# Optimization experiments

Hardware: AMD Instinct MI355X
Metric: run time of the kernel (lower is better)

## Reference

```python
import jax, jax.numpy as jnp
import numpy as np

MASK_PENALTY = 10000.0

def setup_inputs() -> dict:
    key = jax.random.key(0)
    kq, kk, kv = jax.random.split(key, 3)
    B, S, D = 8, 2048, 64
    return {
        "query": jax.random.normal(kq, (B, S, D), dtype=jnp.float32),
        "key": jax.random.normal(kk, (B, S, D), dtype=jnp.float32),
        "value": jax.random.normal(kv, (B, S, D), dtype=jnp.float32),
        "mask": jnp.ones((B, S), dtype=jnp.bool_),
    }

def reference(query, key, value, mask):
    # e: [B, Sq, Sk]
    d = query.shape[-1]
    e = jnp.einsum('bqd,bkd->bqk', query, key) / jnp.sqrt(jnp.float32(d))
    Sq, Sk = query.shape[1], key.shape[1]
    # history_only causal mask: key index > query index gets -10000
    causal = (jnp.arange(Sk)[None, :] > jnp.arange(Sq)[:, None]).astype(jnp.float32)
    e = e - MASK_PENALTY * causal[None, :, :]
    # padding mask: [B, Sk] -> [B, 1, Sk]
    e = e - MASK_PENALTY * (1.0 - mask.astype(jnp.float32))[:, None, :]
    attn = jax.nn.softmax(e, axis=-1)
    return jnp.einsum('bqk,bkd->bqd', attn, value)
```

## Files before the change

### kernel.cpp

```cpp
#include <hip/hip_runtime.h>


typedef _Float16 f16x8 __attribute__((ext_vector_type(8)));
typedef _Float16 f16x4 __attribute__((ext_vector_type(4)));
typedef float    f32x4 __attribute__((ext_vector_type(4)));

#define MFMA_K32(A, B, C) __builtin_amdgcn_mfma_f32_16x16x32_f16(A, B, C, 0, 0, 0)
#define MFMA_K16(A, B, C) __builtin_amdgcn_mfma_f32_16x16x16f16(A, B, C, 0, 0, 0)

__device__ inline unsigned pack2h(float a, float b) {
    union { _Float16 h[2]; unsigned u; } t;
    t.h[0] = (_Float16)a; t.h[1] = (_Float16)b;
    return t.u;
}

constexpr float CSCALE = 0.18033688011112042f;

__global__ __launch_bounds__(256, 4)
void prep_f16(const float* __restrict__ K, const float* __restrict__ V,
              const int* __restrict__ M, _Float16* __restrict__ Kh,
              _Float16* __restrict__ Vq, unsigned char* __restrict__ Mb) {
    __shared__ _Float16 sT[64 * 80];
    const int b   = blockIdx.x >> 5;
    const int s0  = (blockIdx.x & 31) * 64;
    const int t   = threadIdx.x;
    const int row = t >> 2;
    const int grp = (t & 3) * 16;
    const size_t base = ((size_t)b * 2048 + s0 + row) * 64 + grp;
    {
        union { _Float16 h[16]; f16x8 v[2]; } o;
        const float* p = K + base;
#pragma unroll
        for (int i = 0; i < 16; i += 4) {
            float4 x = *(const float4*)(p + i);
            o.h[i]   = (_Float16)(x.x * CSCALE); o.h[i+1] = (_Float16)(x.y * CSCALE);
            o.h[i+2] = (_Float16)(x.z * CSCALE); o.h[i+3] = (_Float16)(x.w * CSCALE);
        }
        *(f16x8*)(Kh + base) = o.v[0];
        *(f16x8*)(Kh + base + 8) = o.v[1];
    }
    {
        const float* p = V + base;
#pragma unroll
        for (int i = 0; i < 16; i += 4) {
            float4 x = *(const float4*)(p + i);
            sT[(grp + i    ) * 80 + row] = (_Float16)x.x;
            sT[(grp + i + 1) * 80 + row] = (_Float16)x.y;
            sT[(grp + i + 2) * 80 + row] = (_Float16)x.z;
            sT[(grp + i + 3) * 80 + row] = (_Float16)x.w;
        }
    }
    if (t < 64) {
        const size_t s = (size_t)b * 2048 + s0 + t;
        Mb[s] = (unsigned char)(M[s] != 0);
    }
    __syncthreads();
    {
        const int d = t & 63, g = t >> 6;
        const size_t o = (((size_t)b * 128 + (s0 >> 4) + g) * 64 + d) * 16;
        *(f16x8*)(Vq + o)     = *(const f16x8*)&sT[d * 80 + g * 16];
        *(f16x8*)(Vq + o + 8) = *(const f16x8*)&sT[d * 80 + g * 16 + 8];
    }
}

constexpr int SOSTR = 68;

__global__ __launch_bounds__(512, 2)
void attn_f16_v6(const float* __restrict__ Q, const _Float16* __restrict__ Kh,
                 const _Float16* __restrict__ Vq, const unsigned char* __restrict__ Mb,
                 float* __restrict__ O) {
    constexpr int S = 2048, D = 64;

    __shared__ float sO[8][32 * SOSTR];
    __shared__ float sL[8][32];

    const int tid  = threadIdx.x;
    const int w    = tid >> 6;
    const int lane = tid & 63;
    const int l15  = lane & 15;
    const int quad = lane >> 4;

    for (int phase = 0; phase < 2; ++phase) {
        const int batch = (int)blockIdx.y ^ phase;
        const int st    = phase ? 63 - (int)blockIdx.x : (int)blockIdx.x;
        const int n_kt  = st + 1;
        const int qg0   = st * 32;
        const size_t bq = (size_t)batch * S;
        const _Float16* Kb = Kh + bq * D;
        const _Float16* Vb = Vq + bq * D;

        f16x8 qf[2][2];
#pragma unroll
        for (int f = 0; f < 2; ++f) {
            const float* qp = Q + (bq + qg0 + f * 16 + l15) * D + quad * 8;
#pragma unroll
            for (int dc = 0; dc < 2; ++dc) {
                float4 x0 = *(const float4*)(qp + dc * 32);
                float4 x1 = *(const float4*)(qp + dc * 32 + 4);
                union { unsigned u[4]; f16x8 v; } t;
                t.u[0] = pack2h(x0.x, x0.y); t.u[1] = pack2h(x0.z, x0.w);
                t.u[2] = pack2h(x1.x, x1.y); t.u[3] = pack2h(x1.z, x1.w);
                qf[f][dc] = t.v;
            }
        }

        f32x4 acc[2][4];
        float lacc[2] = {0.f, 0.f};
#pragma unroll
        for (int f = 0; f < 2; ++f)
#pragma unroll
            for (int c = 0; c < 4; ++c) { acc[f][c][0] = acc[f][c][1] = acc[f][c][2] = acc[f][c][3] = 0.f; }

        f16x8 kn[2][2];
        if (w < n_kt) {
            const int kb = w * 32;
#pragma unroll
            for (int kg = 0; kg < 2; ++kg)
#pragma unroll
                for (int dc = 0; dc < 2; ++dc)
                    kn[kg][dc] = *(const f16x8*)(Kb + (size_t)(kb + kg * 16 + l15) * D + dc * 32 + quad * 8);
        }

        for (int t = w; t < n_kt; t += 8) {
            const int kb = t * 32;

            f16x4 vf[2][4];
#pragma unroll
            for (int kg = 0; kg < 2; ++kg)
#pragma unroll
                for (int c = 0; c < 4; ++c)
                    vf[kg][c] = *(const f16x4*)(Vb + ((size_t)((kb >> 4) + kg) * 64 + c * 16 + l15) * 16 + quad * 4);
            const unsigned um0 = *(const unsigned*)(Mb + bq + kb + quad * 4);
            const unsigned um1 = *(const unsigned*)(Mb + bq + kb + 16 + quad * 4);

            f32x4 scT[2][2];
#pragma unroll
            for (int f = 0; f < 2; ++f) {
                f32x4 z; z[0] = z[1] = z[2] = z[3] = 0.f;
                f32x4 y0 = MFMA_K32(kn[0][0], qf[f][0], z);
                scT[f][0] = MFMA_K32(kn[0][1], qf[f][1], y0);
                f32x4 y1 = MFMA_K32(kn[1][0], qf[f][0], z);
                scT[f][1] = MFMA_K32(kn[1][1], qf[f][1], y1);
            }

            if (t + 8 < n_kt) {
                const int kb2 = kb + 256;
#pragma unroll
                for (int kg = 0; kg < 2; ++kg)
#pragma unroll
                    for (int dc = 0; dc < 2; ++dc)
                        kn[kg][dc] = *(const f16x8*)(Kb + (size_t)(kb2 + kg * 16 + l15) * D + dc * 32 + quad * 8);
            }

#pragma unroll
            for (int f = 0; f < 2; ++f) {
                const int qrow = qg0 + f * 16 + l15;
                f16x4 pf0, pf1;
                {
                    union { _Float16 h[4]; f16x4 v; } pp;
#pragma unroll
                    for (int r = 0; r < 4; ++r) {
                        const int key = kb + quad * 4 + r;
                        float e  = __builtin_amdgcn_exp2f(scT[f][0][r]);
                        bool  ok = (key <= qrow) && (((um0 >> (8 * r)) & 0xFF) != 0);
                        float pv = ok ? e : 0.f;
                        lacc[f] += pv;
                        pp.h[r] = (_Float16)pv;
                    }
                    pf0 = pp.v;
#pragma unroll
                    for (int r = 0; r < 4; ++r) {
                        const int key = kb + 16 + quad * 4 + r;
                        float e  = __builtin_amdgcn_exp2f(scT[f][1][r]);
                        bool  ok = (key <= qrow) && (((um1 >> (8 * r)) & 0xFF) != 0);
                        float pv = ok ? e : 0.f;
                        lacc[f] += pv;
                        pp.h[r] = (_Float16)pv;
                    }
                    pf1 = pp.v;
                }
                acc[f][0] = MFMA_K16(pf0, vf[0][0], acc[f][0]);
                acc[f][1] = MFMA_K16(pf0, vf[0][1], acc[f][1]);
                acc[f][2] = MFMA_K16(pf0, vf[0][2], acc[f][2]);
                acc[f][3] = MFMA_K16(pf0, vf[0][3], acc[f][3]);
                acc[f][0] = MFMA_K16(pf1, vf[1][0], acc[f][0]);
                acc[f][1] = MFMA_K16(pf1, vf[1][1], acc[f][1]);
                acc[f][2] = MFMA_K16(pf1, vf[1][2], acc[f][2]);
                acc[f][3] = MFMA_K16(pf1, vf[1][3], acc[f][3]);
            }
        }

#pragma unroll
        for (int f = 0; f < 2; ++f) {
            lacc[f] += __shfl_xor(lacc[f], 16, 64);
            lacc[f] += __shfl_xor(lacc[f], 32, 64);
        }

#pragma unroll
        for (int f = 0; f < 2; ++f)
#pragma unroll
            for (int c = 0; c < 4; ++c)
#pragma unroll
                for (int r = 0; r < 4; ++r)
                    sO[w][(f * 16 + quad * 4 + r) * SOSTR + c * 16 + l15] = acc[f][c][r];
        if (lane < 16) { sL[w][l15] = lacc[0]; sL[w][16 + l15] = lacc[1]; }
        __syncthreads();
        {
            const int row = tid >> 4;
            const int col = (tid & 15) * 4;
            float a0 = 0.f, a1 = 0.f, a2 = 0.f, a3 = 0.f, l = 0.f;
#pragma unroll
            for (int w2 = 0; w2 < 8; ++w2) {
                const float* p = &sO[w2][row * SOSTR + col];
                a0 += p[0]; a1 += p[1]; a2 += p[2]; a3 += p[3];
                l  += sL[w2][row];
            }
            const float inv = 1.f / fmaxf(l, 1e-37f);
            float4 o; o.x = a0 * inv; o.y = a1 * inv; o.z = a2 * inv; o.w = a3 * inv;
            *(float4*)(&O[(bq + qg0 + row) * D + col]) = o;
        }
        __syncthreads();
    }
}

constexpr int PSTR = 40;
__global__ __launch_bounds__(512, 4)
void attn_f16_slow(const float* __restrict__ Q, const float* __restrict__ K,
                   const float* __restrict__ V, const int* __restrict__ M,
                   float* __restrict__ O) {
    constexpr int S = 2048, D = 64;
    __shared__ __align__(16) _Float16 sP[8][16 * PSTR];
    __shared__ float sO[8][16 * 64];
    __shared__ float sL[8][16];
    const int tid = threadIdx.x, w = tid >> 6, lane = tid & 63;
    const int l15 = lane & 15, quad = lane >> 4;
    for (int phase = 0; phase < 2; ++phase) {
        const int batch = (int)blockIdx.y ^ phase;
        const int tile  = phase ? 127 - (int)blockIdx.x : (int)blockIdx.x;
        const int n_kt  = tile / 2 + 1;
        const int qg0   = tile * 16;
        const size_t bq = (size_t)batch * S;
        f16x8 qf[2];
        {
            const float* qp = Q + (bq + qg0 + l15) * D + quad * 8;
#pragma unroll
            for (int dc = 0; dc < 2; ++dc) {
                float4 x0 = *(const float4*)(qp + dc * 32);
                float4 x1 = *(const float4*)(qp + dc * 32 + 4);
                union { unsigned u[4]; f16x8 v; } t;
                t.u[0] = pack2h(x0.x, x0.y); t.u[1] = pack2h(x0.z, x0.w);
                t.u[2] = pack2h(x1.x, x1.y); t.u[3] = pack2h(x1.z, x1.w);
                qf[dc] = t.v;
            }
        }
        f32x4 acc[4]; float lacc[4];
#pragma unroll
        for (int c = 0; c < 4; ++c) { acc[c][0] = acc[c][1] = acc[c][2] = acc[c][3] = 0.f; }
#pragma unroll
        for (int r = 0; r < 4; ++r) lacc[r] = 0.f;
        for (int t = w; t < n_kt; t += 8) {
            const int kb = t * 32;
            f16x8 kf[2][2];
            {
                const float* kp = K + (bq + kb + l15) * D + quad * 8;
#pragma unroll
                for (int kg = 0; kg < 2; ++kg)
#pragma unroll
                    for (int dc = 0; dc < 2; ++dc) {
                        float4 x0 = *(const float4*)(kp + kg * 16 * D + dc * 32);
                        float4 x1 = *(const float4*)(kp + kg * 16 * D + dc * 32 + 4);
                        union { unsigned u[4]; f16x8 v; } tt;
                        tt.u[0] = pack2h(x0.x * CSCALE, x0.y * CSCALE);
                        tt.u[1] = pack2h(x0.z * CSCALE, x0.w * CSCALE);
                        tt.u[2] = pack2h(x1.x * CSCALE, x1.y * CSCALE);
                        tt.u[3] = pack2h(x1.z * CSCALE, x1.w * CSCALE);
                        kf[kg][dc] = tt.v;
                    }
            }
            float vr[4][8];
            {
                const float* vp = V + (bq + kb + quad * 8) * D + l15;
#pragma unroll
                for (int c = 0; c < 4; ++c)
#pragma unroll
                    for (int j = 0; j < 8; ++j)
                        vr[c][j] = vp[j * D + c * 16];
            }
            const int m0 = M[bq + kb + l15];
            const int m1 = M[bq + kb + 16 + l15];
            f32x4 sc[2];
#pragma unroll
            for (int kg = 0; kg < 2; ++kg) {
                f32x4 z; z[0] = z[1] = z[2] = z[3] = 0.f;
                z = MFMA_K32(qf[0], kf[kg][0], z);
                sc[kg] = MFMA_K32(qf[1], kf[kg][1], z);
            }
            float p[2][4];
#pragma unroll
            for (int kg = 0; kg < 2; ++kg) {
                const int key = kb + kg * 16 + l15;
                const int mv  = kg ? m1 : m0;
#pragma unroll
                for (int r = 0; r < 4; ++r) {
                    const int qrow = qg0 + quad * 4 + r;
                    float e  = __builtin_amdgcn_exp2f(sc[kg][r]);
                    bool  ok = (key <= qrow) && (mv != 0);
                    float pv = ok ? e : 0.f;
                    p[kg][r] = pv;
                    lacc[r] += pv;
                }
            }
            _Float16* sPw = sP[w];
#pragma unroll
            for (int kg = 0; kg < 2; ++kg)
#pragma unroll
                for (int r = 0; r < 4; ++r)
                    sPw[(quad * 4 + r) * PSTR + kg * 16 + l15] = (_Float16)p[kg][r];
            f16x8 pf = *(const f16x8*)(&sPw[l15 * PSTR + quad * 8]);
#pragma unroll
            for (int c = 0; c < 4; ++c) {
                union { unsigned u[4]; f16x8 v; } tt;
                tt.u[0] = pack2h(vr[c][0], vr[c][1]);
                tt.u[1] = pack2h(vr[c][2], vr[c][3]);
                tt.u[2] = pack2h(vr[c][4], vr[c][5]);
                tt.u[3] = pack2h(vr[c][6], vr[c][7]);
                acc[c] = MFMA_K32(pf, tt.v, acc[c]);
            }
        }
#pragma unroll
        for (int r = 0; r < 4; ++r) {
            float s = lacc[r];
            s += __shfl_xor(s, 1, 64);
            s += __shfl_xor(s, 2, 64);
            s += __shfl_xor(s, 4, 64);
            s += __shfl_xor(s, 8, 64);
            lacc[r] = s;
        }
#pragma unroll
        for (int c = 0; c < 4; ++c)
#pragma unroll
            for (int r = 0; r < 4; ++r)
                sO[w][(quad * 4 + r) * 64 + c * 16 + l15] = acc[c][r];
        if (l15 == 0) {
#pragma unroll
            for (int r = 0; r < 4; ++r) sL[w][quad * 4 + r] = lacc[r];
        }
        __syncthreads();
        {
            const int row = tid >> 5;
            const int col = (tid & 31) * 2;
            float a = 0.f, b = 0.f, l = 0.f;
#pragma unroll
            for (int w2 = 0; w2 < 8; ++w2) {
                a += sO[w2][row * 64 + col];
                b += sO[w2][row * 64 + col + 1];
                l += sL[w2][row];
            }
            const float inv = 1.f / fmaxf(l, 1e-37f);
            float2 o; o.x = a * inv; o.y = b * inv;
            *(float2*)(&O[(bq + qg0 + row) * D + col]) = o;
        }
        __syncthreads();
    }
}

extern "C" void kernel_launch(void* const* d_in, const int* in_sizes, int n_in,
                              void* d_out, int out_size, void* d_ws, size_t ws_size,
                              hipStream_t stream) {
    const float* Q = (const float*)d_in[0];
    const float* K = (const float*)d_in[1];
    const float* V = (const float*)d_in[2];
    const int*   M = (const int*)d_in[3];
    float*       O = (float*)d_out;
    const size_t n_kv = (size_t)8 * 2048 * 64;
    const size_t need = n_kv * 2 * sizeof(_Float16) + 8 * 2048;
    if (ws_size >= need) {
        _Float16* Kh = (_Float16*)d_ws;
        _Float16* Vq = Kh + n_kv;
        unsigned char* Mb = (unsigned char*)(Vq + n_kv);
        hipLaunchKernelGGL(prep_f16, dim3(256), dim3(256), 0, stream, K, V, M, Kh, Vq, Mb);
        hipLaunchKernelGGL(attn_f16_v6, dim3(32, 8), dim3(512), 0, stream, Q, Kh, Vq, Mb, O);
    } else {
        hipLaunchKernelGGL(attn_f16_slow, dim3(64, 8), dim3(512), 0, stream, Q, K, V, M, O);
    }
}
```

Before: 85.76 us.

## Double-buffer K/V/mask tiles in registers and use additive float mask bias

Replaces the single K-prefetch with two register slots holding K, V and mask for alternating tiles, so loads for the next-next tile overlap compute on the current one. The padding mask becomes a precomputed additive float bias (0 or -1e5) folded into the exp2 argument, removing the per-element byte extraction and compare. The causal compare now runs only on diagonal tiles. This raises register pressure under launch bounds of 512x2, which could cause spills or lower occupancy.

```diff
diff --git a/kernel.cpp b/kernel.cpp
--- a/kernel.cpp
+++ b/kernel.cpp
@@ -19,7 +19,7 @@
 __global__ __launch_bounds__(256, 4)
 void prep_f16(const float* __restrict__ K, const float* __restrict__ V,
               const int* __restrict__ M, _Float16* __restrict__ Kh,
-              _Float16* __restrict__ Vq, unsigned char* __restrict__ Mb) {
+              _Float16* __restrict__ Vq, float* __restrict__ Mf) {
     __shared__ _Float16 sT[64 * 80];
     const int b   = blockIdx.x >> 5;
     const int s0  = (blockIdx.x & 31) * 64;
@@ -52,7 +52,7 @@
     }
     if (t < 64) {
         const size_t s = (size_t)b * 2048 + s0 + t;
-        Mb[s] = (unsigned char)(M[s] != 0);
+        Mf[s] = M[s] ? 0.f : -1.0e5f;
     }
     __syncthreads();
     {
@@ -65,9 +65,15 @@
 
 constexpr int SOSTR = 68;
 
+struct Slot {
+    f16x8 kf[2][2];
+    f16x4 vf[2][4];
+    float mb[2][4];
+};
+
 __global__ __launch_bounds__(512, 2)
-void attn_f16_v6(const float* __restrict__ Q, const _Float16* __restrict__ Kh,
-                 const _Float16* __restrict__ Vq, const unsigned char* __restrict__ Mb,
+void attn_f16_v7(const float* __restrict__ Q, const _Float16* __restrict__ Kh,
+                 const _Float16* __restrict__ Vq, const float* __restrict__ Mf,
                  float* __restrict__ O) {
     constexpr int S = 2048, D = 64;
 
@@ -88,6 +94,7 @@
         const size_t bq = (size_t)batch * S;
         const _Float16* Kb = Kh + bq * D;
         const _Float16* Vb = Vq + bq * D;
+        const float*    Mb = Mf + bq;
 
         f16x8 qf[2][2];
 #pragma unroll
@@ -111,82 +118,82 @@
 #pragma unroll
             for (int c = 0; c < 4; ++c) { acc[f][c][0] = acc[f][c][1] = acc[f][c][2] = acc[f][c][3] = 0.f; }
 
-        f16x8 kn[2][2];
-        if (w < n_kt) {
-            const int kb = w * 32;
+        auto fill = [&](Slot& s, int kb) {
 #pragma unroll
             for (int kg = 0; kg < 2; ++kg)
 #pragma unroll
                 for (int dc = 0; dc < 2; ++dc)
-                    kn[kg][dc] = *(const f16x8*)(Kb + (size_t)(kb + kg * 16 + l15) * D + dc * 32 + quad * 8);
-        }
-
-        for (int t = w; t < n_kt; t += 8) {
-            const int kb = t * 32;
-
-            f16x4 vf[2][4];
+                    s.kf[kg][dc] = *(const f16x8*)(Kb + (size_t)(kb + kg * 16 + l15) * D + dc * 32 + quad * 8);
 #pragma unroll
             for (int kg = 0; kg < 2; ++kg)
 #pragma unroll
                 for (int c = 0; c < 4; ++c)
-                    vf[kg][c] = *(const f16x4*)(Vb + ((size_t)((kb >> 4) + kg) * 64 + c * 16 + l15) * 16 + quad * 4);
-            const unsigned um0 = *(const unsigned*)(Mb + bq + kb + quad * 4);
-            const unsigned um1 = *(const unsigned*)(Mb + bq + kb + 16 + quad * 4);
-
+                    s.vf[kg][c] = *(const f16x4*)(Vb + ((size_t)((kb >> 4) + kg) * 64 + c * 16 + l15) * 16 + quad * 4);
+#pragma unroll
+            for (int kg = 0; kg < 2; ++kg) {
+                float4 m = *(const float4*)(Mb + kb + kg * 16 + quad * 4);
+                s.mb[kg][0] = m.x; s.mb[kg][1] = m.y; s.mb[kg][2] = m.z; s.mb[kg][3] = m.w;
+            }
+        };
+
+        auto compute_tile = [&](const Slot& s, int kb) {
             f32x4 scT[2][2];
 #pragma unroll
             for (int f = 0; f < 2; ++f) {
                 f32x4 z; z[0] = z[1] = z[2] = z[3] = 0.f;
-                f32x4 y0 = MFMA_K32(kn[0][0], qf[f][0], z);
-                scT[f][0] = MFMA_K32(kn[0][1], qf[f][1], y0);
-                f32x4 y1 = MFMA_K32(kn[1][0], qf[f][0], z);
-                scT[f][1] = MFMA_K32(kn[1][1], qf[f][1], y1);
-            }
-
-            if (t + 8 < n_kt) {
-                const int kb2 = kb + 256;
-#pragma unroll
-                for (int kg = 0; kg < 2; ++kg)
-#pragma unroll
-                    for (int dc = 0; dc < 2; ++dc)
-                        kn[kg][dc] = *(const f16x8*)(Kb + (size_t)(kb2 + kg * 16 + l15) * D + dc * 32 + quad * 8);
-            }
-
+                f32x4 y0 = MFMA_K32(s.kf[0][0], qf[f][0], z);
+                scT[f][0] = MFMA_K32(s.kf[0][1], qf[f][1], y0);
+                f32x4 y1 = MFMA_K32(s.kf[1][0], qf[f][0], z);
+                scT[f][1] = MFMA_K32(s.kf[1][1], qf[f][1], y1);
+            }
+            const bool causal = (kb + 32 > qg0);
 #pragma unroll
             for (int f = 0; f < 2; ++f) {
                 const int qrow = qg0 + f * 16 + l15;
                 f16x4 pf0, pf1;
-                {
-                    union { _Float16 h[4]; f16x4 v; } pp;
-#pragma unroll
-                    for (int r = 0; r < 4; ++r) {
+                union { _Float16 h[4]; f16x4 v; } pp;
+#pragma unroll
+                for (int r = 0; r < 4; ++r) {
+                    float e = __builtin_amdgcn_exp2f(scT[f][0][r] + s.mb[0][r]);
+                    if (causal) {
                         const int key = kb + quad * 4 + r;
-                        float e  = __builtin_amdgcn_exp2f(scT[f][0][r]);
-                        bool  ok = (key <= qrow) && (((um0 >> (8 * r)) & 0xFF) != 0);
-                        float pv = ok ? e : 0.f;
-                        lacc[f] += pv;
-                        pp.h[r] = (_Float16)pv;
+                        e = (key <= qrow) ? e : 0.f;
                     }
-                    pf0 = pp.v;
-#pragma unroll
-                    for (int r = 0; r < 4; ++r) {
+                    lacc[f] += e;
+                    pp.h[r] = (_Float16)e;
+                }
+                pf0 = pp.v;
+#pragma unroll
+                for (int r = 0; r < 4; ++r) {
+                    float e = __builtin_amdgcn_exp2f(scT[f][1][r] + s.mb[1][r]);
+                    if (causal) {
                         const int key = kb + 16 + quad * 4 + r;
-                        float e  = __builtin_amdgcn_exp2f(scT[f][1][r]);
-                        bool  ok = (key <= qrow) && (((um1 >> (8 * r)) & 0xFF) != 0);
-                        float pv = ok ? e : 0.f;
-                        lacc[f] += pv;
-                        pp.h[r] = (_Float16)pv;
+                        e = (key <= qrow) ? e : 0.f;
                     }
-                    pf1 = pp.v;
+                    lacc[f] += e;
+                    pp.h[r] = (_Float16)e;
                 }
-                acc[f][0] = MFMA_K16(pf0, vf[0][0], acc[f][0]);
-                acc[f][1] = MFMA_K16(pf0, vf[0][1], acc[f][1]);
-                acc[f][2] = MFMA_K16(pf0, vf[0][2], acc[f][2]);
-                acc[f][3] = MFMA_K16(pf0, vf[0][3], acc[f][3]);
-                acc[f][0] = MFMA_K16(pf1, vf[1][0], acc[f][0]);
-                acc[f][1] = MFMA_K16(pf1, vf[1][1], acc[f][1]);
-                acc[f][2] = MFMA_K16(pf1, vf[1][2], acc[f][2]);
-                acc[f][3] = MFMA_K16(pf1, vf[1][3], acc[f][3]);
+                pf1 = pp.v;
+                acc[f][0] = MFMA_K16(pf0, s.vf[0][0], acc[f][0]);
+                acc[f][1] = MFMA_K16(pf0, s.vf[0][1], acc[f][1]);
+                acc[f][2] = MFMA_K16(pf0, s.vf[0][2], acc[f][2]);
+                acc[f][3] = MFMA_K16(pf0, s.vf[0][3], acc[f][3]);
+                acc[f][0] = MFMA_K16(pf1, s.vf[1][0], acc[f][0]);
+                acc[f][1] = MFMA_K16(pf1, s.vf[1][1], acc[f][1]);
+                acc[f][2] = MFMA_K16(pf1, s.vf[1][2], acc[f][2]);
+                acc[f][3] = MFMA_K16(pf1, s.vf[1][3], acc[f][3]);
+            }
+        };
+
+        Slot s0, s1;
+        if (w < n_kt)     fill(s0, w * 32);
+        if (w + 8 < n_kt) fill(s1, (w + 8) * 32);
+        for (int t = w; t < n_kt; t += 16) {
+            compute_tile(s0, t * 32);
+            if (t + 16 < n_kt) fill(s0, (t + 16) * 32);
+            if (t + 8 < n_kt) {
+                compute_tile(s1, (t + 8) * 32);
+                if (t + 24 < n_kt) fill(s1, (t + 24) * 32);
             }
         }
 
@@ -373,13 +380,13 @@
     const int*   M = (const int*)d_in[3];
     float*       O = (float*)d_out;
     const size_t n_kv = (size_t)8 * 2048 * 64;
-    const size_t need = n_kv * 2 * sizeof(_Float16) + 8 * 2048;
+    const size_t need = n_kv * 2 * sizeof(_Float16) + (size_t)8 * 2048 * sizeof(float);
     if (ws_size >= need) {
         _Float16* Kh = (_Float16*)d_ws;
         _Float16* Vq = Kh + n_kv;
-        unsigned char* Mb = (unsigned char*)(Vq + n_kv);
-        hipLaunchKernelGGL(prep_f16, dim3(256), dim3(256), 0, stream, K, V, M, Kh, Vq, Mb);
-        hipLaunchKernelGGL(attn_f16_v6, dim3(32, 8), dim3(512), 0, stream, Q, Kh, Vq, Mb, O);
+        float*    Mf = (float*)(Vq + n_kv);
+        hipLaunchKernelGGL(prep_f16, dim3(256), dim3(256), 0, stream, K, V, M, Kh, Vq, Mf);
+        hipLaunchKernelGGL(attn_f16_v7, dim3(32, 8), dim3(512), 0, stream, Q, Kh, Vq, Mf, O);
     } else {
         hipLaunchKernelGGL(attn_f16_slow, dim3(64, 8), dim3(512), 0, stream, Q, K, V, M, O);
     }
```

New measurement: 88.26 us. +2.9%, slower.

## Split attention into 16-row query tiles with 4 waves and additive mask bias

Applied to the files above, without the earlier changes.

Replaces the two-phase paired 32-row blocks of 8 waves with 1024 independent 256-thread blocks. Each block handles 16 query rows, ordered longest-first so the causal load balances across more, smaller blocks. The padding mask becomes a precomputed float additive bias folded into the exponent, and the causal compare runs only on diagonal tiles. This cuts per-element masking ALU work and raises occupancy, at the cost of reloading K/V for every 16 rows instead of every 32 and a larger mask buffer.

```diff
diff --git a/kernel.cpp b/kernel.cpp
--- a/kernel.cpp
+++ b/kernel.cpp
@@ -19,7 +19,7 @@
 __global__ __launch_bounds__(256, 4)
 void prep_f16(const float* __restrict__ K, const float* __restrict__ V,
               const int* __restrict__ M, _Float16* __restrict__ Kh,
-              _Float16* __restrict__ Vq, unsigned char* __restrict__ Mb) {
+              _Float16* __restrict__ Vq, float* __restrict__ Mf) {
     __shared__ _Float16 sT[64 * 80];
     const int b   = blockIdx.x >> 5;
     const int s0  = (blockIdx.x & 31) * 64;
@@ -52,7 +52,7 @@
     }
     if (t < 64) {
         const size_t s = (size_t)b * 2048 + s0 + t;
-        Mb[s] = (unsigned char)(M[s] != 0);
+        Mf[s] = M[s] ? 0.f : -1.0e5f;
     }
     __syncthreads();
     {
@@ -65,14 +65,14 @@
 
 constexpr int SOSTR = 68;
 
-__global__ __launch_bounds__(512, 2)
-void attn_f16_v6(const float* __restrict__ Q, const _Float16* __restrict__ Kh,
-                 const _Float16* __restrict__ Vq, const unsigned char* __restrict__ Mb,
+__global__ __launch_bounds__(256, 4)
+void attn_f16_v8(const float* __restrict__ Q, const _Float16* __restrict__ Kh,
+                 const _Float16* __restrict__ Vq, const float* __restrict__ Mf,
                  float* __restrict__ O) {
     constexpr int S = 2048, D = 64;
 
-    __shared__ float sO[8][32 * SOSTR];
-    __shared__ float sL[8][32];
+    __shared__ float sO[4][16 * SOSTR];
+    __shared__ float sL[4][16];
 
     const int tid  = threadIdx.x;
     const int w    = tid >> 6;
@@ -80,146 +80,139 @@
     const int l15  = lane & 15;
     const int quad = lane >> 4;
 
-    for (int phase = 0; phase < 2; ++phase) {
-        const int batch = (int)blockIdx.y ^ phase;
-        const int st    = phase ? 63 - (int)blockIdx.x : (int)blockIdx.x;
-        const int n_kt  = st + 1;
-        const int qg0   = st * 32;
-        const size_t bq = (size_t)batch * S;
-        const _Float16* Kb = Kh + bq * D;
-        const _Float16* Vb = Vq + bq * D;
-
-        f16x8 qf[2][2];
-#pragma unroll
-        for (int f = 0; f < 2; ++f) {
-            const float* qp = Q + (bq + qg0 + f * 16 + l15) * D + quad * 8;
-#pragma unroll
-            for (int dc = 0; dc < 2; ++dc) {
-                float4 x0 = *(const float4*)(qp + dc * 32);
-                float4 x1 = *(const float4*)(qp + dc * 32 + 4);
-                union { unsigned u[4]; f16x8 v; } t;
-                t.u[0] = pack2h(x0.x, x0.y); t.u[1] = pack2h(x0.z, x0.w);
-                t.u[2] = pack2h(x1.x, x1.y); t.u[3] = pack2h(x1.z, x1.w);
-                qf[f][dc] = t.v;
-            }
-        }
-
-        f32x4 acc[2][4];
-        float lacc[2] = {0.f, 0.f};
-#pragma unroll
-        for (int f = 0; f < 2; ++f)
-#pragma unroll
-            for (int c = 0; c < 4; ++c) { acc[f][c][0] = acc[f][c][1] = acc[f][c][2] = acc[f][c][3] = 0.f; }
-
-        f16x8 kn[2][2];
-        if (w < n_kt) {
-            const int kb = w * 32;
+    const int idx   = (int)blockIdx.x;
+    const int tile  = 127 - (idx >> 3);
+    const int batch = idx & 7;
+    const int n_kt  = tile / 2 + 1;
+    const int qg0   = tile * 16;
+    const size_t bq = (size_t)batch * S;
+    const _Float16* Kb = Kh + bq * D;
+    const _Float16* Vb = Vq + bq * D;
+    const float*    Mb = Mf + bq;
+
+    f16x8 qf[2];
+    {
+        const float* qp = Q + (bq + qg0 + l15) * D + quad * 8;
+#pragma unroll
+        for (int dc = 0; dc < 2; ++dc) {
+            float4 x0 = *(const float4*)(qp + dc * 32);
+            float4 x1 = *(const float4*)(qp + dc * 32 + 4);
+            union { unsigned u[4]; f16x8 v; } t;
+            t.u[0] = pack2h(x0.x, x0.y); t.u[1] = pack2h(x0.z, x0.w);
+            t.u[2] = pack2h(x1.x, x1.y); t.u[3] = pack2h(x1.z, x1.w);
+            qf[dc] = t.v;
+        }
+    }
+
+    f32x4 acc[4];
+    float lacc = 0.f;
+#pragma unroll
+    for (int c = 0; c < 4; ++c) { acc[c][0] = acc[c][1] = acc[c][2] = acc[c][3] = 0.f; }
+
+    f16x8 kn[2][2];
+    if (w < n_kt) {
+        const int kb = w * 32;
+#pragma unroll
+        for (int kg = 0; kg < 2; ++kg)
+#pragma unroll
+            for (int dc = 0; dc < 2; ++dc)
+                kn[kg][dc] = *(const f16x8*)(Kb + (size_t)(kb + kg * 16 + l15) * D + dc * 32 + quad * 8);
+    }
+
+    for (int t = w; t < n_kt; t += 4) {
+        const int kb = t * 32;
+
+        f16x4 vf[2][4];
+#pragma unroll
+        for (int kg = 0; kg < 2; ++kg)
+#pragma unroll
+            for (int c = 0; c < 4; ++c)
+                vf[kg][c] = *(const f16x4*)(Vb + ((size_t)((kb >> 4) + kg) * 64 + c * 16 + l15) * 16 + quad * 4);
+        float4 mbias0 = *(const float4*)(Mb + kb + quad * 4);
+        float4 mbias1 = *(const float4*)(Mb + kb + 16 + quad * 4);
+
+        f32x4 scT0, scT1;
+        {
+            f32x4 z; z[0] = z[1] = z[2] = z[3] = 0.f;
+            f32x4 y0 = MFMA_K32(kn[0][0], qf[0], z);
+            scT0 = MFMA_K32(kn[0][1], qf[1], y0);
+            f32x4 y1 = MFMA_K32(kn[1][0], qf[0], z);
+            scT1 = MFMA_K32(kn[1][1], qf[1], y1);
+        }
+
+        if (t + 4 < n_kt) {
+            const int kb2 = kb + 128;
 #pragma unroll
             for (int kg = 0; kg < 2; ++kg)
 #pragma unroll
                 for (int dc = 0; dc < 2; ++dc)
-                    kn[kg][dc] = *(const f16x8*)(Kb + (size_t)(kb + kg * 16 + l15) * D + dc * 32 + quad * 8);
-        }
-
-        for (int t = w; t < n_kt; t += 8) {
-            const int kb = t * 32;
-
-            f16x4 vf[2][4];
-#pragma unroll
-            for (int kg = 0; kg < 2; ++kg)
-#pragma unroll
-                for (int c = 0; c < 4; ++c)
-                    vf[kg][c] = *(const f16x4*)(Vb + ((size_t)((kb >> 4) + kg) * 64 + c * 16 + l15) * 16 + quad * 4);
-            const unsigned um0 = *(const unsigned*)(Mb + bq + kb + quad * 4);
-            const unsigned um1 = *(const unsigned*)(Mb + bq + kb + 16 + quad * 4);
-
-            f32x4 scT[2][2];
-#pragma unroll
-            for (int f = 0; f < 2; ++f) {
-                f32x4 z; z[0] = z[1] = z[2] = z[3] = 0.f;
-                f32x4 y0 = MFMA_K32(kn[0][0], qf[f][0], z);
-                scT[f][0] = MFMA_K32(kn[0][1], qf[f][1], y0);
-                f32x4 y1 = MFMA_K32(kn[1][0], qf[f][0], z);
-                scT[f][1] = MFMA_K32(kn[1][1], qf[f][1], y1);
-            }
-
-            if (t + 8 < n_kt) {
-                const int kb2 = kb + 256;
-#pragma unroll
-                for (int kg = 0; kg < 2; ++kg)
-#pragma unroll
-                    for (int dc = 0; dc < 2; ++dc)
-                        kn[kg][dc] = *(const f16x8*)(Kb + (size_t)(kb2 + kg * 16 + l15) * D + dc * 32 + quad * 8);
-            }
-
-#pragma unroll
-            for (int f = 0; f < 2; ++f) {
-                const int qrow = qg0 + f * 16 + l15;
-                f16x4 pf0, pf1;
-                {
-                    union { _Float16 h[4]; f16x4 v; } pp;
-#pragma unroll
-                    for (int r = 0; r < 4; ++r) {
-                        const int key = kb + quad * 4 + r;
-                        float e  = __builtin_amdgcn_exp2f(scT[f][0][r]);
-                        bool  ok = (key <= qrow) && (((um0 >> (8 * r)) & 0xFF) != 0);
-                        float pv = ok ? e : 0.f;
-                        lacc[f] += pv;
-                        pp.h[r] = (_Float16)pv;
-                    }
-                    pf0 = pp.v;
-#pragma unroll
-                    for (int r = 0; r < 4; ++r) {
-                        const int key = kb + 16 + quad * 4 + r;
-                        float e  = __builtin_amdgcn_exp2f(scT[f][1][r]);
-                        bool  ok = (key <= qrow) && (((um1 >> (8 * r)) & 0xFF) != 0);
-                        float pv = ok ? e : 0.f;
-                        lacc[f] += pv;
-                        pp.h[r] = (_Float16)pv;
-                    }
-                    pf1 = pp.v;
+                    kn[kg][dc] = *(const f16x8*)(Kb + (size_t)(kb2 + kg * 16 + l15) * D + dc * 32 + quad * 8);
+        }
+
+        const bool diag = (kb + 32 > qg0);
+        const int qrow = qg0 + l15;
+        f16x4 pf0, pf1;
+        {
+            union { _Float16 h[4]; f16x4 v; } pp;
+            const float mb0[4] = {mbias0.x, mbias0.y, mbias0.z, mbias0.w};
+#pragma unroll
+            for (int r = 0; r < 4; ++r) {
+                float e = __builtin_amdgcn_exp2f(scT0[r] + mb0[r]);
+                if (diag) {
+                    const int key = kb + quad * 4 + r;
+                    e = (key <= qrow) ? e : 0.f;
                 }
-                acc[f][0] = MFMA_K16(pf0, vf[0][0], acc[f][0]);
-                acc[f][1] = MFMA_K16(pf0, vf[0][1], acc[f][1]);
-                acc[f][2] = MFMA_K16(pf0, vf[0][2], acc[f][2]);
-                acc[f][3] = MFMA_K16(pf0, vf[0][3], acc[f][3]);
-                acc[f][0] = MFMA_K16(pf1, vf[1][0], acc[f][0]);
-                acc[f][1] = MFMA_K16(pf1, vf[1][1], acc[f][1]);
-                acc[f][2] = MFMA_K16(pf1, vf[1][2], acc[f][2]);
-                acc[f][3] = MFMA_K16(pf1, vf[1][3], acc[f][3]);
-            }
-        }
-
-#pragma unroll
-        for (int f = 0; f < 2; ++f) {
-            lacc[f] += __shfl_xor(lacc[f], 16, 64);
-            lacc[f] += __shfl_xor(lacc[f], 32, 64);
-        }
-
-#pragma unroll
-        for (int f = 0; f < 2; ++f)
-#pragma unroll
-            for (int c = 0; c < 4; ++c)
-#pragma unroll
-                for (int r = 0; r < 4; ++r)
-                    sO[w][(f * 16 + quad * 4 + r) * SOSTR + c * 16 + l15] = acc[f][c][r];
-        if (lane < 16) { sL[w][l15] = lacc[0]; sL[w][16 + l15] = lacc[1]; }
-        __syncthreads();
-        {
-            const int row = tid >> 4;
-            const int col = (tid & 15) * 4;
-            float a0 = 0.f, a1 = 0.f, a2 = 0.f, a3 = 0.f, l = 0.f;
-#pragma unroll
-            for (int w2 = 0; w2 < 8; ++w2) {
-                const float* p = &sO[w2][row * SOSTR + col];
-                a0 += p[0]; a1 += p[1]; a2 += p[2]; a3 += p[3];
-                l  += sL[w2][row];
-            }
-            const float inv = 1.f / fmaxf(l, 1e-37f);
-            float4 o; o.x = a0 * inv; o.y = a1 * inv; o.z = a2 * inv; o.w = a3 * inv;
-            *(float4*)(&O[(bq + qg0 + row) * D + col]) = o;
-        }
-        __syncthreads();
+                lacc += e;
+                pp.h[r] = (_Float16)e;
+            }
+            pf0 = pp.v;
+            const float mb1[4] = {mbias1.x, mbias1.y, mbias1.z, mbias1.w};
+#pragma unroll
+            for (int r = 0; r < 4; ++r) {
+                float e = __builtin_amdgcn_exp2f(scT1[r] + mb1[r]);
+                if (diag) {
+                    const int key = kb + 16 + quad * 4 + r;
+                    e = (key <= qrow) ? e : 0.f;
+                }
+                lacc += e;
+                pp.h[r] = (_Float16)e;
+            }
+            pf1 = pp.v;
+        }
+
+        acc[0] = MFMA_K16(pf0, vf[0][0], acc[0]);
+        acc[1] = MFMA_K16(pf0, vf[0][1], acc[1]);
+        acc[2] = MFMA_K16(pf0, vf[0][2], acc[2]);
+        acc[3] = MFMA_K16(pf0, vf[0][3], acc[3]);
+        acc[0] = MFMA_K16(pf1, vf[1][0], acc[0]);
+        acc[1] = MFMA_K16(pf1, vf[1][1], acc[1]);
+        acc[2] = MFMA_K16(pf1, vf[1][2], acc[2]);
+        acc[3] = MFMA_K16(pf1, vf[1][3], acc[3]);
+    }
+
+    lacc += __shfl_xor(lacc, 16, 64);
+    lacc += __shfl_xor(lacc, 32, 64);
+
+#pragma unroll
+    for (int c = 0; c < 4; ++c)
+#pragma unroll
+        for (int r = 0; r < 4; ++r)
+            sO[w][(quad * 4 + r) * SOSTR + c * 16 + l15] = acc[c][r];
+    if (lane < 16) sL[w][l15] = lacc;
+    __syncthreads();
+    {
+        const int row = tid >> 4;
+        const int col = (tid & 15) * 4;
+        float a0 = 0.f, a1 = 0.f, a2 = 0.f, a3 = 0.f, l = 0.f;
+#pragma unroll
+        for (int w2 = 0; w2 < 4; ++w2) {
+            const float* p = &sO[w2][row * SOSTR + col];
+            a0 += p[0]; a1 += p[1]; a2 += p[2]; a3 += p[3];
+            l  += sL[w2][row];
+        }
+        const float inv = 1.f / fmaxf(l, 1e-37f);
+        float4 o; o.x = a0 * inv; o.y = a1 * inv; o.z = a2 * inv; o.w = a3 * inv;
+        *(float4*)(&O[(bq + qg0 + row) * D + col]) = o;
     }
 }
 
@@ -373,13 +366,13 @@
     const int*   M = (const int*)d_in[3];
     float*       O = (float*)d_out;
     const size_t n_kv = (size_t)8 * 2048 * 64;
-    const size_t need = n_kv * 2 * sizeof(_Float16) + 8 * 2048;
+    const size_t need = n_kv * 2 * sizeof(_Float16) + (size_t)8 * 2048 * sizeof(float);
     if (ws_size >= need) {
         _Float16* Kh = (_Float16*)d_ws;
         _Float16* Vq = Kh + n_kv;
-        unsigned char* Mb = (unsigned char*)(Vq + n_kv);
-        hipLaunchKernelGGL(prep_f16, dim3(256), dim3(256), 0, stream, K, V, M, Kh, Vq, Mb);
-        hipLaunchKernelGGL(attn_f16_v6, dim3(32, 8), dim3(512), 0, stream, Q, Kh, Vq, Mb, O);
+        float*    Mf = (float*)(Vq + n_kv);
+        hipLaunchKernelGGL(prep_f16, dim3(256), dim3(256), 0, stream, K, V, M, Kh, Vq, Mf);
+        hipLaunchKernelGGL(attn_f16_v8, dim3(1024), dim3(256), 0, stream, Q, Kh, Vq, Mf, O);
     } else {
         hipLaunchKernelGGL(attn_f16_slow, dim3(64, 8), dim3(512), 0, stream, Q, K, V, M, O);
     }
```

New measurement: 101.0 us. +17.7%, slower.
